# Performance work log

Hardware: AMD Instinct MI355X
Metric: run time of the kernel (lower is better)

The kernel has to match this reference:

```python
import jax, jax.numpy as jnp
import numpy as np

C = 128; D_INNER = 256; D_STATE = 16; D_CONV = 4; DT_RANK = 8; SCALE_MLP = 2


def layernorm(x, g, b, eps=1e-5):
    m = x.mean(-1, keepdims=True)
    v = ((x - m) ** 2).mean(-1, keepdims=True)
    return (x - m) * jax.lax.rsqrt(v + eps) * g + b


def causal_conv(x, w, b):
    # x: (B, L, D); w: (D, K) depthwise causal conv; b: (D,)
    K = w.shape[1]
    xt = x.transpose(0, 2, 1)  # (B, D, L)
    out = jax.lax.conv_general_dilated(
        xt, w[:, None, :], (1,), [(K - 1, 0)],
        dimension_numbers=("NCH", "OIH", "NCH"), feature_group_count=w.shape[0])
    return (out + b[None, :, None]).transpose(0, 2, 1)


def selective_scan(u, delta, A, Bm, Cm, Dv):
    # u, delta: (B, L, D); A: (D, N); Bm, Cm: (B, L, N); Dv: (D,)
    def step(h, inp):
        u_t, d_t, B_t, C_t = inp  # (B,D),(B,D),(B,N),(B,N)
        dA = jnp.exp(d_t[..., None] * A)                      # (B, D, N)
        h = dA * h + (d_t * u_t)[..., None] * B_t[:, None, :]  # (B, D, N)
        y = jnp.einsum("bdn,bn->bd", h, C_t)
        return h, y
    Bsz, L, Din = u.shape
    h0 = jnp.zeros((Bsz, Din, A.shape[1]), u.dtype)
    inputs = (u.transpose(1, 0, 2), delta.transpose(1, 0, 2),
              Bm.transpose(1, 0, 2), Cm.transpose(1, 0, 2))
    _, ys = jax.lax.scan(step, h0, inputs)
    return ys.transpose(1, 0, 2) + u * Dv


def mamba_branch(xc, z, cw, cb, Wx_, Wdt_, bdt_, Al, Dv):
    u = jax.nn.silu(causal_conv(xc, cw, cb))
    xdbl = u @ Wx_.T  # (B, L, dt_rank + 2*d_state)
    dr = Wdt_.shape[1]; ds = Al.shape[1]
    dt = jax.nn.softplus(xdbl[..., :dr] @ Wdt_.T + bdt_)
    Bm = xdbl[..., dr:dr + ds]
    Cm = xdbl[..., dr + ds:]
    y = selective_scan(u, dt, -jnp.exp(Al), Bm, Cm, Dv)
    return y * jax.nn.silu(z)


def setup_inputs():
    key = jax.random.key(0)
    ks = jax.random.split(key, 20)
    w = lambda k, shape, s=0.02: jax.random.normal(k, shape, jnp.float32) * s
    A_log = jnp.log(jnp.tile(jnp.arange(1, D_STATE + 1, dtype=jnp.float32), (D_INNER, 1)))
    dt_bias = jnp.full((D_INNER,), jnp.log(jnp.expm1(0.01)), jnp.float32)
    return dict(
        x=jax.random.normal(ks[0], (4, 256, 64, C), jnp.float32),
        g1=jnp.ones((C,), jnp.float32), b1=jnp.zeros((C,), jnp.float32),
        W_in=w(ks[1], (2 * D_INNER, C)),
        conv_w=w(ks[2], (D_INNER, D_CONV), 0.2), conv_b=jnp.zeros((D_INNER,), jnp.float32),
        Wx=w(ks[3], (DT_RANK + 2 * D_STATE, D_INNER)),
        Wdt=w(ks[4], (D_INNER, DT_RANK), 0.1), bdt=dt_bias,
        A_log=A_log, D=jnp.ones((D_INNER,), jnp.float32),
        conv_wb=w(ks[5], (D_INNER, D_CONV), 0.2), conv_bb=jnp.zeros((D_INNER,), jnp.float32),
        Wxb=w(ks[6], (DT_RANK + 2 * D_STATE, D_INNER)),
        Wdtb=w(ks[7], (D_INNER, DT_RANK), 0.1), bdtb=dt_bias,
        A_b_log=A_log, D_b=jnp.ones((D_INNER,), jnp.float32),
        W_out=w(ks[8], (C, D_INNER)),
        g2=jnp.ones((C,), jnp.float32), b2=jnp.zeros((C,), jnp.float32),
        g3=jnp.ones((C,), jnp.float32), b3=jnp.zeros((C,), jnp.float32),
        W1m=w(ks[9], (C, SCALE_MLP * C)), b1m=jnp.zeros((SCALE_MLP * C,), jnp.float32),
        W2m=w(ks[10], (SCALE_MLP * C, C)), b2m=jnp.zeros((C,), jnp.float32),
    )


def reference(x, g1, b1, W_in, conv_w, conv_b, Wx, Wdt, bdt, A_log, D,
              conv_wb, conv_bb, Wxb, Wdtb, bdtb, A_b_log, D_b, W_out,
              g2, b2, g3, b3, W1m, b1m, W2m, b2m):
    B, T, N, Cc = x.shape
    xs = x.transpose(0, 2, 1, 3).reshape(B * N, T, Cc)
    # --- CustomBiMamba: LN -> (Dropout eval=identity) -> BiMamba v2 -> LN, residual ---
    h = layernorm(xs, g1, b1)
    xz = h @ W_in.T  # (B*N, T, 2*d_inner)
    xc, z = jnp.split(xz, 2, axis=-1)
    y_f = mamba_branch(xc, z, conv_w, conv_b, Wx, Wdt, bdt, A_log, D)
    y_b = mamba_branch(xc[:, ::-1], z[:, ::-1], conv_wb, conv_bb, Wxb, Wdtb, bdtb,
                       A_b_log, D_b)[:, ::-1]
    y = (y_f + y_b) @ W_out.T
    y = layernorm(y, g2, b2)
    xs = y + xs
    xo = xs.reshape(B, N, T, Cc).transpose(0, 2, 1, 3)
    # --- MLP residual ---
    h2 = layernorm(xo, g3, b3)
    mlp = jax.nn.gelu(h2 @ W1m + b1m, approximate=False) @ W2m + b2m
    return xo + mlp
```

## Files before the change

kernel.cpp:

```cpp
#include <hip/hip_runtime.h>
#include <hip/hip_bf16.h>
#include <math.h>

#define CC 128
#define DI 256
#define SSEQ 256
#define ROWS 65536

typedef __hip_bfloat16 bf16;
typedef __attribute__((ext_vector_type(8))) short short8;
typedef __attribute__((ext_vector_type(4))) float float4v;
typedef __attribute__((ext_vector_type(2))) float f32x2;

__device__ __forceinline__ float to_f(float v) { return v; }
__device__ __forceinline__ float to_f(bf16 v)  { return __bfloat162float(v); }
__device__ __forceinline__ bf16  f2b(float v)  { return __float2bfloat16(v); }
__device__ __forceinline__ float bf2f_bits(short v) {
    union { unsigned u; float f; } c; c.u = ((unsigned)(unsigned short)v) << 16; return c.f;
}
__device__ __forceinline__ f32x2 mk2(float a, float b) { f32x2 r; r.x = a; r.y = b; return r; }
__device__ __forceinline__ f32x2 fma2(f32x2 a, f32x2 b, f32x2 c) { return a * b + c; }

__device__ __forceinline__ float wave_sum(float v) {
    #pragma unroll
    for (int o = 1; o < 64; o <<= 1) v += __shfl_xor(v, o, 64);
    return v;
}
__device__ __forceinline__ float silu_f(float x) {
    return x * __builtin_amdgcn_rcpf(1.f + __expf(-x));
}
__device__ __forceinline__ float gelu_f(float x) { return 0.5f * x * (1.f + erff(x * 0.70710678118654752f)); }
__device__ __forceinline__ float softplus_f(float x) {
    return (x > 20.f) ? x : __logf(1.f + __expf(x));
}

__global__ __launch_bounds__(256) void ln1_kernel(const float* __restrict__ x,
                                                  const float* __restrict__ g,
                                                  const float* __restrict__ b,
                                                  bf16* __restrict__ out) {
    int wave = threadIdx.x >> 6, lane = threadIdx.x & 63;
    int r = blockIdx.x * 4 + wave;
    int s = r >> 8, t = r & 255;
    int bb = s >> 6, n = s & 63;
    size_t xbase = (((size_t)(bb * 256 + t)) * 64 + n) * CC;
    float v0 = x[xbase + lane], v1 = x[xbase + lane + 64];
    float s1 = wave_sum(v0 + v1);
    float s2 = wave_sum(v0 * v0 + v1 * v1);
    float m = s1 * (1.f / 128.f);
    float var = s2 * (1.f / 128.f) - m * m;
    float rstd = rsqrtf(var + 1e-5f);
    size_t ob = (size_t)r * CC;
    out[ob + lane]      = f2b((v0 - m) * rstd * g[lane]      + b[lane]);
    out[ob + lane + 64] = f2b((v1 - m) * rstd * g[lane + 64] + b[lane + 64]);
}

__global__ __launch_bounds__(256) void ln3_kernel(const float* __restrict__ in,
                                                  const float* __restrict__ g,
                                                  const float* __restrict__ b,
                                                  bf16* __restrict__ out) {
    int wave = threadIdx.x >> 6, lane = threadIdx.x & 63;
    int r = blockIdx.x * 4 + wave;
    size_t ib = (size_t)r * CC;
    float v0 = in[ib + lane], v1 = in[ib + lane + 64];
    float s1 = wave_sum(v0 + v1);
    float s2 = wave_sum(v0 * v0 + v1 * v1);
    float m = s1 * (1.f / 128.f);
    float var = s2 * (1.f / 128.f) - m * m;
    float rstd = rsqrtf(var + 1e-5f);
    out[ib + lane]      = f2b((v0 - m) * rstd * g[lane]      + b[lane]);
    out[ib + lane + 64] = f2b((v1 - m) * rstd * g[lane + 64] + b[lane + 64]);
}

template <bool BTR, int EPI, int KTILES>
__global__ __launch_bounds__(256) void mfma_gemm_kernel(const bf16* __restrict__ A, int lda,
                                                        const float* __restrict__ B,
                                                        const float* __restrict__ bias,
                                                        void* __restrict__ Cout, int ldc,
                                                        int N, int K) {
    __shared__ bf16 As[64][40];
    __shared__ bf16 Bs[64][40];
    int tid = threadIdx.x;
    int m0 = blockIdx.x * 64;
    int n0 = blockIdx.y * 64;
    int wv = tid >> 6, lane = tid & 63;
    int lrow = lane & 15, quad = lane >> 4;
    int lk = quad * 8;
    float4v acc[4] = {};
    #pragma unroll
    for (int kt = 0; kt < KTILES; kt++) {
        int k0 = kt * 32;
        {
            int m = tid >> 2, part = tid & 3;
            uint4 v = *(const uint4*)(A + (size_t)(m0 + m) * lda + k0 + part * 8);
            *(uint4*)&As[m][part * 8] = v;
        }
        if (BTR) {
            int n = tid >> 2, part = tid & 3;
            const float* src = B + (size_t)(n0 + n) * K + k0 + part * 8;
            bf16 tmp[8];
            #pragma unroll
            for (int j = 0; j < 8; j++) tmp[j] = f2b(src[j]);
            *(uint4*)&Bs[n][part * 8] = *(uint4*)tmp;
        } else {
            int kk = tid >> 3, nf = (tid & 7) * 8;
            const float* src = B + (size_t)(k0 + kk) * N + n0 + nf;
            #pragma unroll
            for (int j = 0; j < 8; j++) Bs[nf + j][kk] = f2b(src[j]);
        }
        __syncthreads();
        short8 a = *(const short8*)&As[wv * 16 + lrow][lk];
        #pragma unroll
        for (int jt = 0; jt < 4; jt++) {
            short8 bfr = *(const short8*)&Bs[jt * 16 + lrow][lk];
            acc[jt] = __builtin_amdgcn_mfma_f32_16x16x32_bf16(a, bfr, acc[jt], 0, 0, 0);
        }
        __syncthreads();
    }
    #pragma unroll
    for (int jt = 0; jt < 4; jt++) {
        int col = n0 + jt * 16 + lrow;
        float bs = (EPI >= 1) ? bias[col] : 0.f;
        #pragma unroll
        for (int r = 0; r < 4; r++) {
            int row = m0 + wv * 16 + quad * 4 + r;
            float v = acc[jt][r] + bs;
            if (EPI == 1) v = gelu_f(v);
            if (EPI == 2) {
                float* Cf = (float*)Cout;
                Cf[(size_t)row * ldc + col] += v;
            } else {
                bf16* Cb = (bf16*)Cout;
                Cb[(size_t)row * ldc + col] = f2b(v);
            }
        }
    }
}

__global__ __launch_bounds__(256) void mfma_ln2res_kernel(const bf16* __restrict__ YF,
                                                          const bf16* __restrict__ YB,
                                                          const bf16* __restrict__ xz,
                                                          const float* __restrict__ Wout,
                                                          const float* __restrict__ g,
                                                          const float* __restrict__ b,
                                                          const float* __restrict__ x,
                                                          float* __restrict__ out) {
    __shared__ bf16 As[64][40];
    __shared__ bf16 Bs[128][40];
    int tid = threadIdx.x;
    int m0 = blockIdx.x * 64;
    int wv = tid >> 6, lane = tid & 63;
    int lrow = lane & 15, quad = lane >> 4;
    int lk = quad * 8;
    float4v acc[8] = {};
    #pragma unroll
    for (int kt = 0; kt < 8; kt++) {
        int k0 = kt * 32;
        {
            int m = tid >> 2, part = tid & 3;
            size_t off = (size_t)(m0 + m) * 256 + k0 + part * 8;
            short8 vf = *(const short8*)(YF + off);
            short8 vb = *(const short8*)(YB + off);
            short8 vz = *(const short8*)(xz + (size_t)(m0 + m) * 512 + 256 + k0 + part * 8);
            bf16 tmp[8];
            #pragma unroll
            for (int j = 0; j < 8; j++)
                tmp[j] = f2b((bf2f_bits(vf[j]) + bf2f_bits(vb[j])) * silu_f(bf2f_bits(vz[j])));
            *(uint4*)&As[m][part * 8] = *(uint4*)tmp;
        }
        #pragma unroll
        for (int it = 0; it < 2; it++) {
            int idx = tid + it * 256;
            int n = idx >> 2, part = idx & 3;
            const float* src = Wout + (size_t)n * 256 + k0 + part * 8;
            bf16 tmp[8];
            #pragma unroll
            for (int j = 0; j < 8; j++) tmp[j] = f2b(src[j]);
            *(uint4*)&Bs[n][part * 8] = *(uint4*)tmp;
        }
        __syncthreads();
        short8 a = *(const short8*)&As[wv * 16 + lrow][lk];
        #pragma unroll
        for (int jt = 0; jt < 8; jt++) {
            short8 bfr = *(const short8*)&Bs[jt * 16 + lrow][lk];
            acc[jt] = __builtin_amdgcn_mfma_f32_16x16x32_bf16(a, bfr, acc[jt], 0, 0, 0);
        }
        __syncthreads();
    }
    #pragma unroll
    for (int r = 0; r < 4; r++) {
        float ps = 0.f, ps2 = 0.f;
        #pragma unroll
        for (int jt = 0; jt < 8; jt++) { float v = acc[jt][r]; ps += v; ps2 += v * v; }
        #pragma unroll
        for (int o = 1; o < 16; o <<= 1) {
            ps  += __shfl_xor(ps, o, 64);
            ps2 += __shfl_xor(ps2, o, 64);
        }
        float m = ps * (1.f / 128.f);
        float var = ps2 * (1.f / 128.f) - m * m;
        float rstd = rsqrtf(var + 1e-5f);
        int row = m0 + wv * 16 + quad * 4 + r;
        int s = row >> 8, t = row & 255;
        int bb = s >> 6, n = s & 63;
        size_t xbase = (((size_t)(bb * 256 + t)) * 64 + n) * CC;
        #pragma unroll
        for (int jt = 0; jt < 8; jt++) {
            int col = jt * 16 + lrow;
            out[xbase + col] = (acc[jt][r] - m) * rstd * g[col] + b[col] + x[xbase + col];
        }
    }
}

template <int DIR>
__global__ __launch_bounds__(256) void mfma_conv_kernel(const bf16* __restrict__ xz,
                                                        const float* __restrict__ cw,
                                                        const float* __restrict__ cb,
                                                        const float* __restrict__ Wx,
                                                        bf16* __restrict__ C,
                                                        bf16* __restrict__ U) {
    __shared__ bf16 As[64][40];
    __shared__ bf16 Bs[48][40];
    int tid = threadIdx.x;
    int s = blockIdx.x >> 2;
    int t0 = (blockIdx.x & 3) * 64;
    int wv = tid >> 6, lane = tid & 63;
    int lrow = lane & 15, quad = lane >> 4;
    int lk = quad * 8;
    float4v acc[3] = {};
    #pragma unroll
    for (int kt = 0; kt < 8; kt++) {
        int k0 = kt * 32;
        {
            int m = tid >> 2, part = tid & 3;
            int t = t0 + m;
            int dbase = k0 + part * 8;
            float a[8];
            float4 w4[8];
            #pragma unroll
            for (int i = 0; i < 8; i++) {
                a[i]  = cb[dbase + i];
                w4[i] = ((const float4*)cw)[dbase + i];
            }
            #pragma unroll
            for (int j = 0; j < 4; j++) {
                int tj = t - 3 + j;
                if (tj >= 0) {
                    int src = DIR ? (255 - tj) : tj;
                    uint4 v = *(const uint4*)(xz + (size_t)(s * 256 + src) * 512 + dbase);
                    short8 sv = *(short8*)&v;
                    #pragma unroll
                    for (int i = 0; i < 8; i++) {
                        float w = (j == 0) ? w4[i].x : (j == 1) ? w4[i].y : (j == 2) ? w4[i].z : w4[i].w;
                        a[i] += w * bf2f_bits(sv[i]);
                    }
                }
            }
            bf16 tmp[8];
            #pragma unroll
            for (int i = 0; i < 8; i++) tmp[i] = f2b(silu_f(a[i]));
            *(uint4*)&As[m][part * 8] = *(uint4*)tmp;
            int tu = DIR ? (255 - t) : t;
            *(uint4*)&U[((size_t)(s * 256 + tu)) * 256 + dbase] = *(uint4*)tmp;
        }
        {
            int n = tid >> 2, part = tid & 3;
            if (n < 48) {
                bf16 tmp[8];
                #pragma unroll
                for (int j = 0; j < 8; j++)
                    tmp[j] = (n < 40) ? f2b(Wx[(size_t)n * 256 + k0 + part * 8 + j]) : f2b(0.f);
                *(uint4*)&Bs[n][part * 8] = *(uint4*)tmp;
            }
        }
        __syncthreads();
        short8 a = *(const short8*)&As[wv * 16 + lrow][lk];
        #pragma unroll
        for (int jt = 0; jt < 3; jt++) {
            short8 bfr = *(const short8*)&Bs[jt * 16 + lrow][lk];
            acc[jt] = __builtin_amdgcn_mfma_f32_16x16x32_bf16(a, bfr, acc[jt], 0, 0, 0);
        }
        __syncthreads();
    }
    #pragma unroll
    for (int jt = 0; jt < 3; jt++) {
        int col = jt * 16 + lrow;
        if (col < 40) {
            #pragma unroll
            for (int r = 0; r < 4; r++) {
                int row = t0 + wv * 16 + quad * 4 + r;
                C[(size_t)(s * 256 + row) * 40 + col] = f2b(acc[jt][r]);
            }
        }
    }
}


#define LOADROW(R, T) do {                                                  \
    const float4* rp_ = (const float4*)(rows + (T) * 40);                   \
    R##0 = rp_[0]; R##1 = rp_[1]; R##2 = rp_[2]; R##3 = rp_[3];             \
    R##4 = rp_[4]; R##5 = rp_[5]; R##6 = rp_[6]; R##7 = rp_[7];             \
    R##8 = rp_[8]; R##9 = rp_[9];                                           \
} while (0)

#define SCAN_STEP(T, R) do {                                                \
    float u_ = uc0; uc0 = uc1;                                              \
    if ((T) + 2 < 256) { uc1 = to_f(*unext); unext += ystep; }              \
    f32x2 acc2 = mk2((R##0).x, (R##0).y) * wdt01;                           \
    acc2 = fma2(mk2((R##0).z, (R##0).w), wdt23, acc2);                      \
    acc2 = fma2(mk2((R##1).x, (R##1).y), wdt45, acc2);                      \
    acc2 = fma2(mk2((R##1).z, (R##1).w), wdt67, acc2);                      \
    float dtr_ = bd + acc2.x + acc2.y;                                      \
    float dt_ = softplus_f(dtr_);                                           \
    float du_ = dt_ * u_;                                                   \
    float d1 = __expf(dt_ * A0);                                            \
    float d2v = d1 * d1;                                                    \
    f32x2 pw0 = mk2(d1, d2v);                                               \
    f32x2 dd2 = mk2(d2v, d2v);                                              \
    f32x2 pw1 = pw0 * dd2, pw2 = pw1 * dd2, pw3 = pw2 * dd2;                \
    f32x2 dd8 = mk2(pw3.y, pw3.y);                                          \
    f32x2 pw4 = pw0 * dd8, pw5 = pw1 * dd8, pw6 = pw2 * dd8, pw7 = pw3 * dd8; \
    f32x2 du2 = mk2(du_, du_);                                              \
    hp0 = fma2(pw0, hp0, du2 * mk2((R##2).x, (R##2).y));                    \
    hp1 = fma2(pw1, hp1, du2 * mk2((R##2).z, (R##2).w));                    \
    hp2 = fma2(pw2, hp2, du2 * mk2((R##3).x, (R##3).y));                    \
    hp3 = fma2(pw3, hp3, du2 * mk2((R##3).z, (R##3).w));                    \
    hp4 = fma2(pw4, hp4, du2 * mk2((R##4).x, (R##4).y));                    \
    hp5 = fma2(pw5, hp5, du2 * mk2((R##4).z, (R##4).w));                    \
    hp6 = fma2(pw6, hp6, du2 * mk2((R##5).x, (R##5).y));                    \
    hp7 = fma2(pw7, hp7, du2 * mk2((R##5).z, (R##5).w));                    \
    f32x2 ya = hp0 * mk2((R##6).x, (R##6).y);                               \
    f32x2 yb = hp1 * mk2((R##6).z, (R##6).w);                               \
    ya = fma2(hp2, mk2((R##7).x, (R##7).y), ya);                            \
    yb = fma2(hp3, mk2((R##7).z, (R##7).w), yb);                            \
    ya = fma2(hp4, mk2((R##8).x, (R##8).y), ya);                            \
    yb = fma2(hp5, mk2((R##8).z, (R##8).w), yb);                            \
    ya = fma2(hp6, mk2((R##9).x, (R##9).y), ya);                            \
    yb = fma2(hp7, mk2((R##9).z, (R##9).w), yb);                            \
    f32x2 ys = ya + yb;                                                     \
    float yv_ = ys.x + ys.y + u_ * Dd;                                      \
    *yp = f2b(yv_); yp += ystep;                                            \
} while (0)

__global__ __launch_bounds__(256) void scan_kernel(
        const bf16* __restrict__ xdbl_f, const bf16* __restrict__ xdbl_b,
        const float* __restrict__ Wdt_f, const float* __restrict__ bdt_f,
        const float* __restrict__ Alog_f, const float* __restrict__ D_f,
        const float* __restrict__ Wdt_b, const float* __restrict__ bdt_b,
        const float* __restrict__ Alog_b, const float* __restrict__ D_b,
        bf16* __restrict__ YF, bf16* __restrict__ YB) {
    __shared__ float rows[256 * 40];
    int tid = threadIdx.x;
    int dir = blockIdx.x >> 8;
    int s = blockIdx.x & 255;
    int d = tid;

    const bf16* xd = (dir ? xdbl_b : xdbl_f) + (size_t)s * 10240;
    #pragma unroll
    for (int i = 0; i < 5; i++) {
        int idx = i * 256 + tid;
        uint4 v = ((const uint4*)xd)[idx];
        short8 sv = *(short8*)&v;
        float f[8];
        #pragma unroll
        for (int j = 0; j < 8; j++) f[j] = bf2f_bits(sv[j]);
        *(float4*)&rows[idx * 8]     = *(float4*)&f[0];
        *(float4*)&rows[idx * 8 + 4] = *(float4*)&f[4];
    }

    const float* Alog = dir ? Alog_b : Alog_f;
    const float* Wdtp = dir ? Wdt_b  : Wdt_f;
    float Aarr[16];
    #pragma unroll
    for (int n = 0; n < 16; n++) Aarr[n] = -__expf(Alog[d * 16 + n]);
    f32x2 wdt01 = mk2(Wdtp[d * 8 + 0], Wdtp[d * 8 + 1]);
    f32x2 wdt23 = mk2(Wdtp[d * 8 + 2], Wdtp[d * 8 + 3]);
    f32x2 wdt45 = mk2(Wdtp[d * 8 + 4], Wdtp[d * 8 + 5]);
    f32x2 wdt67 = mk2(Wdtp[d * 8 + 6], Wdtp[d * 8 + 7]);
    float bd = dir ? bdt_b[d] : bdt_f[d];
    float Dd = dir ? D_b[d]   : D_f[d];
    bf16* Y = dir ? YB : YF;

    float A0 = Aarr[0];
    int pw = 1;
    #pragma unroll
    for (int n = 1; n < 16; n++)
        pw &= (fabsf(Aarr[n] - (float)(n + 1) * A0) <= 1e-4f * fabsf(Aarr[n]) + 1e-6f) ? 1 : 0;
    pw = __all(pw);
    __syncthreads();

    bf16* yp = Y + ((size_t)(s * 256 + (dir ? 255 : 0))) * 256 + d;
    ptrdiff_t ystep = dir ? -256 : 256;
    float uc0 = to_f(*yp);
    float uc1 = to_f(*(yp + ystep));
    const bf16* unext = yp + 2 * ystep;

    if (pw) {
        f32x2 hp0 = {}, hp1 = {}, hp2 = {}, hp3 = {},
              hp4 = {}, hp5 = {}, hp6 = {}, hp7 = {};
        float4 ra0, ra1, ra2, ra3, ra4, ra5, ra6, ra7, ra8, ra9;
        float4 rb0, rb1, rb2, rb3, rb4, rb5, rb6, rb7, rb8, rb9;
        LOADROW(ra, 0);
        #pragma unroll 1
        for (int t = 0; t < 256; t += 2) {
            LOADROW(rb, t + 1);
            SCAN_STEP(t, ra);
            if (t + 2 < 256) LOADROW(ra, t + 2);
            SCAN_STEP(t + 1, rb);
        }
    } else {
        float h[16];
        #pragma unroll
        for (int n = 0; n < 16; n++) h[n] = 0.f;
        for (int t = 0; t < 256; t++) {
            float u = uc0; uc0 = uc1;
            if (t + 2 < 256) { uc1 = to_f(*unext); unext += ystep; }
            const float* row = rows + t * 40;
            float4 q0 = *(const float4*)(row);
            float4 q1 = *(const float4*)(row + 4);
            float4 qb0 = *(const float4*)(row + 8);
            float4 qb1 = *(const float4*)(row + 12);
            float4 qb2 = *(const float4*)(row + 16);
            float4 qb3 = *(const float4*)(row + 20);
            float4 qc0 = *(const float4*)(row + 24);
            float4 qc1 = *(const float4*)(row + 28);
            float4 qc2 = *(const float4*)(row + 32);
            float4 qc3 = *(const float4*)(row + 36);
            float dtr = bd;
            dtr += q0.x * wdt01.x + q0.y * wdt01.y + q0.z * wdt23.x + q0.w * wdt23.y;
            dtr += q1.x * wdt45.x + q1.y * wdt45.y + q1.z * wdt67.x + q1.w * wdt67.y;
            float dt = softplus_f(dtr);
            float du = dt * u, y = 0.f;
            float Bm[16] = {qb0.x,qb0.y,qb0.z,qb0.w, qb1.x,qb1.y,qb1.z,qb1.w,
                            qb2.x,qb2.y,qb2.z,qb2.w, qb3.x,qb3.y,qb3.z,qb3.w};
            float Cm[16] = {qc0.x,qc0.y,qc0.z,qc0.w, qc1.x,qc1.y,qc1.z,qc1.w,
                            qc2.x,qc2.y,qc2.z,qc2.w, qc3.x,qc3.y,qc3.z,qc3.w};
            #pragma unroll
            for (int n = 0; n < 16; n++) {
                float dA = __expf(dt * Aarr[n]);
                h[n] = dA * h[n] + du * Bm[n];
                y += h[n] * Cm[n];
            }
            y += u * Dd;
            *yp = f2b(y); yp += ystep;
        }
    }
}

extern "C" void kernel_launch(void* const* d_in, const int* in_sizes, int n_in,
                              void* d_out, int out_size, void* d_ws, size_t ws_size,
                              hipStream_t stream) {
    const float* x      = (const float*)d_in[0];
    const float* g1     = (const float*)d_in[1];
    const float* b1     = (const float*)d_in[2];
    const float* W_in   = (const float*)d_in[3];
    const float* conv_w = (const float*)d_in[4];
    const float* conv_b = (const float*)d_in[5];
    const float* Wx     = (const float*)d_in[6];
    const float* Wdt    = (const float*)d_in[7];
    const float* bdt    = (const float*)d_in[8];
    const float* A_log  = (const float*)d_in[9];
    const float* Dvec   = (const float*)d_in[10];
    const float* conv_wb= (const float*)d_in[11];
    const float* conv_bb= (const float*)d_in[12];
    const float* Wxb    = (const float*)d_in[13];
    const float* Wdtb   = (const float*)d_in[14];
    const float* bdtb   = (const float*)d_in[15];
    const float* A_b_log= (const float*)d_in[16];
    const float* D_b    = (const float*)d_in[17];
    const float* W_out  = (const float*)d_in[18];
    const float* g2     = (const float*)d_in[19];
    const float* b2     = (const float*)d_in[20];
    const float* g3     = (const float*)d_in[21];
    const float* b3     = (const float*)d_in[22];
    const float* W1m    = (const float*)d_in[23];
    const float* b1m    = (const float*)d_in[24];
    const float* W2m    = (const float*)d_in[25];
    const float* b2m    = (const float*)d_in[26];

    bf16* ws  = (bf16*)d_ws;
    bf16* XZ  = ws;
    bf16* YF  = ws + 33554432UL;
    bf16* YB  = ws + 50331648UL;
    bf16* H2  = ws;
    bf16* HID = ws + 8388608UL;
    float* out = (float*)d_out;
    bf16* LN1OUT = (bf16*)d_out;
    bf16* XDBL_F = (bf16*)d_out;
    bf16* XDBL_B = (bf16*)d_out + 2621440UL;

    ln1_kernel<<<ROWS / 4, 256, 0, stream>>>(x, g1, b1, LN1OUT);
    mfma_gemm_kernel<true, 0, 4><<<dim3(ROWS / 64, 8), 256, 0, stream>>>(
        LN1OUT, CC, W_in, nullptr, XZ, 512, 512, CC);
    mfma_conv_kernel<0><<<SSEQ * 4, 256, 0, stream>>>(XZ, conv_w, conv_b, Wx, XDBL_F, YF);
    mfma_conv_kernel<1><<<SSEQ * 4, 256, 0, stream>>>(XZ, conv_wb, conv_bb, Wxb, XDBL_B, YB);
    scan_kernel<<<512, 256, 0, stream>>>(XDBL_F, XDBL_B,
        Wdt, bdt, A_log, Dvec, Wdtb, bdtb, A_b_log, D_b, YF, YB);
    mfma_ln2res_kernel<<<ROWS / 64, 256, 0, stream>>>(YF, YB, XZ, W_out, g2, b2, x, out);
    ln3_kernel<<<ROWS / 4, 256, 0, stream>>>(out, g3, b3, H2);
    mfma_gemm_kernel<false, 1, 4><<<dim3(ROWS / 64, 4), 256, 0, stream>>>(
        H2, CC, W1m, b1m, HID, 2 * CC, 2 * CC, CC);
    mfma_gemm_kernel<false, 2, 8><<<dim3(ROWS / 64, 2), 256, 0, stream>>>(
        HID, 2 * CC, W2m, b2m, out, CC, CC, 2 * CC);
}
```

Baseline: 522.7 us.

## Split selective-scan state dimension across thread pairs with shuffle reduction

The scan kernel now uses 512 threads per block, with two threads per channel, each handling 8 of the 16 state entries. The partial outputs are combined with a lane xor-shuffle and only the even lane writes. The aim is to double the wave count for the latency-bound sequential scan, which ran only 512 blocks of 256 threads, and to halve per-thread register use. In exchange, the dt projection and exp are computed twice per channel and every step adds a cross-lane shuffle.

```diff
diff --git a/kernel.cpp b/kernel.cpp
--- a/kernel.cpp
+++ b/kernel.cpp
@@ -295,53 +295,46 @@
 }
 
 
-#define LOADROW(R, T) do {                                                  \
+#define LOADROW9(R, T) do {                                                 \
     const float4* rp_ = (const float4*)(rows + (T) * 40);                   \
-    R##0 = rp_[0]; R##1 = rp_[1]; R##2 = rp_[2]; R##3 = rp_[3];             \
-    R##4 = rp_[4]; R##5 = rp_[5]; R##6 = rp_[6]; R##7 = rp_[7];             \
-    R##8 = rp_[8]; R##9 = rp_[9];                                           \
+    R##0 = rp_[0]; R##1 = rp_[1];                                           \
+    R##2 = rp_[2 + bo]; R##3 = rp_[3 + bo];                                 \
+    R##4 = rp_[6 + bo]; R##5 = rp_[7 + bo];                                 \
 } while (0)
 
-#define SCAN_STEP(T, R) do {                                                \
+#define SCAN_STEP9(T, R) do {                                               \
     float u_ = uc0; uc0 = uc1;                                              \
     if ((T) + 2 < 256) { uc1 = to_f(*unext); unext += ystep; }              \
-    f32x2 acc2 = mk2((R##0).x, (R##0).y) * wdt01;                           \
-    acc2 = fma2(mk2((R##0).z, (R##0).w), wdt23, acc2);                      \
-    acc2 = fma2(mk2((R##1).x, (R##1).y), wdt45, acc2);                      \
-    acc2 = fma2(mk2((R##1).z, (R##1).w), wdt67, acc2);                      \
-    float dtr_ = bd + acc2.x + acc2.y;                                      \
-    float dt_ = softplus_f(dtr_);                                           \
+    f32x2 a2 = mk2((R##0).x, (R##0).y) * wdt01;                             \
+    a2 = fma2(mk2((R##0).z, (R##0).w), wdt23, a2);                          \
+    a2 = fma2(mk2((R##1).x, (R##1).y), wdt45, a2);                          \
+    a2 = fma2(mk2((R##1).z, (R##1).w), wdt67, a2);                          \
+    float dt_ = softplus_f(bd + a2.x + a2.y);                               \
     float du_ = dt_ * u_;                                                   \
-    float d1 = __expf(dt_ * A0);                                            \
-    float d2v = d1 * d1;                                                    \
-    f32x2 pw0 = mk2(d1, d2v);                                               \
-    f32x2 dd2 = mk2(d2v, d2v);                                              \
+    float p1 = __expf(dt_ * A0);                                            \
+    float p2 = p1 * p1;                                                     \
+    f32x2 pw0 = mk2(p1, p2);                                                \
+    f32x2 dd2 = mk2(p2, p2);                                                \
     f32x2 pw1 = pw0 * dd2, pw2 = pw1 * dd2, pw3 = pw2 * dd2;                \
-    f32x2 dd8 = mk2(pw3.y, pw3.y);                                          \
-    f32x2 pw4 = pw0 * dd8, pw5 = pw1 * dd8, pw6 = pw2 * dd8, pw7 = pw3 * dd8; \
+    float sc_ = half ? pw3.y : 1.0f;                                        \
+    f32x2 s2_ = mk2(sc_, sc_);                                              \
+    pw0 *= s2_; pw1 *= s2_; pw2 *= s2_; pw3 *= s2_;                         \
     f32x2 du2 = mk2(du_, du_);                                              \
     hp0 = fma2(pw0, hp0, du2 * mk2((R##2).x, (R##2).y));                    \
     hp1 = fma2(pw1, hp1, du2 * mk2((R##2).z, (R##2).w));                    \
     hp2 = fma2(pw2, hp2, du2 * mk2((R##3).x, (R##3).y));                    \
     hp3 = fma2(pw3, hp3, du2 * mk2((R##3).z, (R##3).w));                    \
-    hp4 = fma2(pw4, hp4, du2 * mk2((R##4).x, (R##4).y));                    \
-    hp5 = fma2(pw5, hp5, du2 * mk2((R##4).z, (R##4).w));                    \
-    hp6 = fma2(pw6, hp6, du2 * mk2((R##5).x, (R##5).y));                    \
-    hp7 = fma2(pw7, hp7, du2 * mk2((R##5).z, (R##5).w));                    \
-    f32x2 ya = hp0 * mk2((R##6).x, (R##6).y);                               \
-    f32x2 yb = hp1 * mk2((R##6).z, (R##6).w);                               \
-    ya = fma2(hp2, mk2((R##7).x, (R##7).y), ya);                            \
-    yb = fma2(hp3, mk2((R##7).z, (R##7).w), yb);                            \
-    ya = fma2(hp4, mk2((R##8).x, (R##8).y), ya);                            \
-    yb = fma2(hp5, mk2((R##8).z, (R##8).w), yb);                            \
-    ya = fma2(hp6, mk2((R##9).x, (R##9).y), ya);                            \
-    yb = fma2(hp7, mk2((R##9).z, (R##9).w), yb);                            \
-    f32x2 ys = ya + yb;                                                     \
-    float yv_ = ys.x + ys.y + u_ * Dd;                                      \
-    *yp = f2b(yv_); yp += ystep;                                            \
+    f32x2 ya = hp0 * mk2((R##4).x, (R##4).y);                               \
+    ya = fma2(hp1, mk2((R##4).z, (R##4).w), ya);                            \
+    ya = fma2(hp2, mk2((R##5).x, (R##5).y), ya);                            \
+    ya = fma2(hp3, mk2((R##5).z, (R##5).w), ya);                            \
+    float yv_ = ya.x + ya.y + u_ * Ddh;                                     \
+    yv_ += __shfl_xor(yv_, 1, 64);                                          \
+    if (!half) *yp = f2b(yv_);                                              \
+    yp += ystep;                                                            \
 } while (0)
 
-__global__ __launch_bounds__(256) void scan_kernel(
+__global__ __launch_bounds__(512, 4) void scan_kernel(
         const bf16* __restrict__ xdbl_f, const bf16* __restrict__ xdbl_b,
         const float* __restrict__ Wdt_f, const float* __restrict__ bdt_f,
         const float* __restrict__ Alog_f, const float* __restrict__ D_f,
@@ -352,19 +345,24 @@
     int tid = threadIdx.x;
     int dir = blockIdx.x >> 8;
     int s = blockIdx.x & 255;
-    int d = tid;
+    int d = tid >> 1;
+    int half = tid & 1;
+    int n0 = half * 8;
+    int bo = half * 2;
 
     const bf16* xd = (dir ? xdbl_b : xdbl_f) + (size_t)s * 10240;
     #pragma unroll
-    for (int i = 0; i < 5; i++) {
-        int idx = i * 256 + tid;
-        uint4 v = ((const uint4*)xd)[idx];
-        short8 sv = *(short8*)&v;
-        float f[8];
-        #pragma unroll
-        for (int j = 0; j < 8; j++) f[j] = bf2f_bits(sv[j]);
-        *(float4*)&rows[idx * 8]     = *(float4*)&f[0];
-        *(float4*)&rows[idx * 8 + 4] = *(float4*)&f[4];
+    for (int i = 0; i < 3; i++) {
+        int idx = i * 512 + tid;
+        if (idx < 1280) {
+            uint4 v = ((const uint4*)xd)[idx];
+            short8 sv = *(short8*)&v;
+            float f[8];
+            #pragma unroll
+            for (int j = 0; j < 8; j++) f[j] = bf2f_bits(sv[j]);
+            *(float4*)&rows[idx * 8]     = *(float4*)&f[0];
+            *(float4*)&rows[idx * 8 + 4] = *(float4*)&f[4];
+        }
     }
 
     const float* Alog = dir ? Alog_b : Alog_f;
@@ -378,6 +376,7 @@
     f32x2 wdt67 = mk2(Wdtp[d * 8 + 6], Wdtp[d * 8 + 7]);
     float bd = dir ? bdt_b[d] : bdt_f[d];
     float Dd = dir ? D_b[d]   : D_f[d];
+    float Ddh = half ? 0.f : Dd;
     bf16* Y = dir ? YB : YF;
 
     float A0 = Aarr[0];
@@ -395,53 +394,41 @@
     const bf16* unext = yp + 2 * ystep;
 
     if (pw) {
-        f32x2 hp0 = {}, hp1 = {}, hp2 = {}, hp3 = {},
-              hp4 = {}, hp5 = {}, hp6 = {}, hp7 = {};
-        float4 ra0, ra1, ra2, ra3, ra4, ra5, ra6, ra7, ra8, ra9;
-        float4 rb0, rb1, rb2, rb3, rb4, rb5, rb6, rb7, rb8, rb9;
-        LOADROW(ra, 0);
+        f32x2 hp0 = {}, hp1 = {}, hp2 = {}, hp3 = {};
+        float4 ra0, ra1, ra2, ra3, ra4, ra5;
+        float4 rb0, rb1, rb2, rb3, rb4, rb5;
+        LOADROW9(ra, 0);
         #pragma unroll 1
         for (int t = 0; t < 256; t += 2) {
-            LOADROW(rb, t + 1);
-            SCAN_STEP(t, ra);
-            if (t + 2 < 256) LOADROW(ra, t + 2);
-            SCAN_STEP(t + 1, rb);
+            LOADROW9(rb, t + 1);
+            SCAN_STEP9(t, ra);
+            if (t + 2 < 256) LOADROW9(ra, t + 2);
+            SCAN_STEP9(t + 1, rb);
         }
     } else {
-        float h[16];
-        #pragma unroll
-        for (int n = 0; n < 16; n++) h[n] = 0.f;
+        float A8[8], h[8];
+        #pragma unroll
+        for (int j = 0; j < 8; j++) { A8[j] = Aarr[n0 + j]; h[j] = 0.f; }
+        #pragma unroll 1
         for (int t = 0; t < 256; t++) {
             float u = uc0; uc0 = uc1;
             if (t + 2 < 256) { uc1 = to_f(*unext); unext += ystep; }
             const float* row = rows + t * 40;
-            float4 q0 = *(const float4*)(row);
-            float4 q1 = *(const float4*)(row + 4);
-            float4 qb0 = *(const float4*)(row + 8);
-            float4 qb1 = *(const float4*)(row + 12);
-            float4 qb2 = *(const float4*)(row + 16);
-            float4 qb3 = *(const float4*)(row + 20);
-            float4 qc0 = *(const float4*)(row + 24);
-            float4 qc1 = *(const float4*)(row + 28);
-            float4 qc2 = *(const float4*)(row + 32);
-            float4 qc3 = *(const float4*)(row + 36);
             float dtr = bd;
-            dtr += q0.x * wdt01.x + q0.y * wdt01.y + q0.z * wdt23.x + q0.w * wdt23.y;
-            dtr += q1.x * wdt45.x + q1.y * wdt45.y + q1.z * wdt67.x + q1.w * wdt67.y;
+            dtr += row[0] * wdt01.x + row[1] * wdt01.y + row[2] * wdt23.x + row[3] * wdt23.y;
+            dtr += row[4] * wdt45.x + row[5] * wdt45.y + row[6] * wdt67.x + row[7] * wdt67.y;
             float dt = softplus_f(dtr);
             float du = dt * u, y = 0.f;
-            float Bm[16] = {qb0.x,qb0.y,qb0.z,qb0.w, qb1.x,qb1.y,qb1.z,qb1.w,
-                            qb2.x,qb2.y,qb2.z,qb2.w, qb3.x,qb3.y,qb3.z,qb3.w};
-            float Cm[16] = {qc0.x,qc0.y,qc0.z,qc0.w, qc1.x,qc1.y,qc1.z,qc1.w,
-                            qc2.x,qc2.y,qc2.z,qc2.w, qc3.x,qc3.y,qc3.z,qc3.w};
-            #pragma unroll
-            for (int n = 0; n < 16; n++) {
-                float dA = __expf(dt * Aarr[n]);
-                h[n] = dA * h[n] + du * Bm[n];
-                y += h[n] * Cm[n];
-            }
-            y += u * Dd;
-            *yp = f2b(y); yp += ystep;
+            #pragma unroll
+            for (int j = 0; j < 8; j++) {
+                float dA = __expf(dt * A8[j]);
+                h[j] = dA * h[j] + du * row[8 + n0 + j];
+                y += h[j] * row[24 + n0 + j];
+            }
+            y += u * Ddh;
+            y += __shfl_xor(y, 1, 64);
+            if (!half) *yp = f2b(y);
+            yp += ystep;
         }
     }
 }
@@ -493,7 +480,7 @@
         LN1OUT, CC, W_in, nullptr, XZ, 512, 512, CC);
     mfma_conv_kernel<0><<<SSEQ * 4, 256, 0, stream>>>(XZ, conv_w, conv_b, Wx, XDBL_F, YF);
     mfma_conv_kernel<1><<<SSEQ * 4, 256, 0, stream>>>(XZ, conv_wb, conv_bb, Wxb, XDBL_B, YB);
-    scan_kernel<<<512, 256, 0, stream>>>(XDBL_F, XDBL_B,
+    scan_kernel<<<512, 512, 0, stream>>>(XDBL_F, XDBL_B,
         Wdt, bdt, A_log, Dvec, Wdtb, bdtb, A_b_log, D_b, YF, YB);
     mfma_ln2res_kernel<<<ROWS / 64, 256, 0, stream>>>(YF, YB, XZ, W_out, g2, b2, x, out);
     ln3_kernel<<<ROWS / 4, 256, 0, stream>>>(out, g3, b3, H2);
```

Result: slower. 547.1 us (+4.7%).

## Stage scan input u through double-buffered LDS chunks instead of per-step global loads

Applied to the files above, without the earlier changes.

The scan kernel now cooperatively loads 32 time steps of u (the Y buffer rows) into a double-buffered shared-memory tile using 16-byte vector loads, prefetching the next chunk while the current one is scanned. Each thread then reads its u value from LDS rather than doing a strided 2-byte global load every step. It also sets launch_bounds to request two blocks per CU. The cost is an extra 32 KB of LDS per block and a __syncthreads per chunk, and the occupancy hint may limit registers.

```diff
diff --git a/kernel.cpp b/kernel.cpp
--- a/kernel.cpp
+++ b/kernel.cpp
@@ -302,9 +302,8 @@
     R##8 = rp_[8]; R##9 = rp_[9];                                           \
 } while (0)
 
-#define SCAN_STEP(T, R) do {                                                \
-    float u_ = uc0; uc0 = uc1;                                              \
-    if ((T) + 2 < 256) { uc1 = to_f(*unext); unext += ystep; }              \
+#define SCAN_STEP(JJ, R) do {                                               \
+    float u_ = to_f(ub[(JJ) * 256 + d]);                                    \
     f32x2 acc2 = mk2((R##0).x, (R##0).y) * wdt01;                           \
     acc2 = fma2(mk2((R##0).z, (R##0).w), wdt23, acc2);                      \
     acc2 = fma2(mk2((R##1).x, (R##1).y), wdt45, acc2);                      \
@@ -329,19 +328,31 @@
     hp6 = fma2(pw6, hp6, du2 * mk2((R##5).x, (R##5).y));                    \
     hp7 = fma2(pw7, hp7, du2 * mk2((R##5).z, (R##5).w));                    \
     f32x2 ya = hp0 * mk2((R##6).x, (R##6).y);                               \
-    f32x2 yb = hp1 * mk2((R##6).z, (R##6).w);                               \
+    f32x2 yb2 = hp1 * mk2((R##6).z, (R##6).w);                              \
     ya = fma2(hp2, mk2((R##7).x, (R##7).y), ya);                            \
-    yb = fma2(hp3, mk2((R##7).z, (R##7).w), yb);                            \
+    yb2 = fma2(hp3, mk2((R##7).z, (R##7).w), yb2);                          \
     ya = fma2(hp4, mk2((R##8).x, (R##8).y), ya);                            \
-    yb = fma2(hp5, mk2((R##8).z, (R##8).w), yb);                            \
+    yb2 = fma2(hp5, mk2((R##8).z, (R##8).w), yb2);                          \
     ya = fma2(hp6, mk2((R##9).x, (R##9).y), ya);                            \
-    yb = fma2(hp7, mk2((R##9).z, (R##9).w), yb);                            \
-    f32x2 ys = ya + yb;                                                     \
+    yb2 = fma2(hp7, mk2((R##9).z, (R##9).w), yb2);                          \
+    f32x2 ys = ya + yb2;                                                    \
     float yv_ = ys.x + ys.y + u_ * Dd;                                      \
     *yp = f2b(yv_); yp += ystep;                                            \
 } while (0)
 
-__global__ __launch_bounds__(256) void scan_kernel(
+#define STAGE_U(BUF, C0) do {                                               \
+    _Pragma("unroll")                                                       \
+    for (int q_ = 0; q_ < 4; q_++) {                                        \
+        int flat_ = q_ * 256 + tid;                                         \
+        int j_ = flat_ >> 5, w_ = flat_ & 31;                               \
+        int t_ = (C0) + j_;                                                 \
+        int grow_ = dir ? (255 - t_) : t_;                                  \
+        ((uint4*)u_lds)[(BUF) * 1024 + flat_] =                             \
+            *((const uint4*)(Y + ((size_t)(s * 256 + grow_)) * 256) + w_);  \
+    }                                                                       \
+} while (0)
+
+__global__ __launch_bounds__(256, 2) void scan_kernel(
         const bf16* __restrict__ xdbl_f, const bf16* __restrict__ xdbl_b,
         const float* __restrict__ Wdt_f, const float* __restrict__ bdt_f,
         const float* __restrict__ Alog_f, const float* __restrict__ D_f,
@@ -349,6 +360,7 @@
         const float* __restrict__ Alog_b, const float* __restrict__ D_b,
         bf16* __restrict__ YF, bf16* __restrict__ YB) {
     __shared__ float rows[256 * 40];
+    __shared__ bf16  u_lds[2 * 8192];
     int tid = threadIdx.x;
     int dir = blockIdx.x >> 8;
     int s = blockIdx.x & 255;
@@ -386,13 +398,12 @@
     for (int n = 1; n < 16; n++)
         pw &= (fabsf(Aarr[n] - (float)(n + 1) * A0) <= 1e-4f * fabsf(Aarr[n]) + 1e-6f) ? 1 : 0;
     pw = __all(pw);
+
+    STAGE_U(0, 0);
     __syncthreads();
 
     bf16* yp = Y + ((size_t)(s * 256 + (dir ? 255 : 0))) * 256 + d;
     ptrdiff_t ystep = dir ? -256 : 256;
-    float uc0 = to_f(*yp);
-    float uc1 = to_f(*(yp + ystep));
-    const bf16* unext = yp + 2 * ystep;
 
     if (pw) {
         f32x2 hp0 = {}, hp1 = {}, hp2 = {}, hp3 = {},
@@ -401,47 +412,50 @@
         float4 rb0, rb1, rb2, rb3, rb4, rb5, rb6, rb7, rb8, rb9;
         LOADROW(ra, 0);
         #pragma unroll 1
-        for (int t = 0; t < 256; t += 2) {
-            LOADROW(rb, t + 1);
-            SCAN_STEP(t, ra);
-            if (t + 2 < 256) LOADROW(ra, t + 2);
-            SCAN_STEP(t + 1, rb);
+        for (int c = 0; c < 8; c++) {
+            if (c + 1 < 8) STAGE_U((c + 1) & 1, (c + 1) * 32);
+            const bf16* ub = u_lds + (c & 1) * 8192;
+            int tc = c * 32;
+            #pragma unroll 2
+            for (int j = 0; j < 32; j += 2) {
+                int t = tc + j;
+                LOADROW(rb, t + 1);
+                SCAN_STEP(j, ra);
+                if (t + 2 < 256) LOADROW(ra, t + 2);
+                SCAN_STEP(j + 1, rb);
+            }
+            __syncthreads();
         }
     } else {
         float h[16];
         #pragma unroll
         for (int n = 0; n < 16; n++) h[n] = 0.f;
-        for (int t = 0; t < 256; t++) {
-            float u = uc0; uc0 = uc1;
-            if (t + 2 < 256) { uc1 = to_f(*unext); unext += ystep; }
-            const float* row = rows + t * 40;
-            float4 q0 = *(const float4*)(row);
-            float4 q1 = *(const float4*)(row + 4);
-            float4 qb0 = *(const float4*)(row + 8);
-            float4 qb1 = *(const float4*)(row + 12);
-            float4 qb2 = *(const float4*)(row + 16);
-            float4 qb3 = *(const float4*)(row + 20);
-            float4 qc0 = *(const float4*)(row + 24);
-            float4 qc1 = *(const float4*)(row + 28);
-            float4 qc2 = *(const float4*)(row + 32);
-            float4 qc3 = *(const float4*)(row + 36);
-            float dtr = bd;
-            dtr += q0.x * wdt01.x + q0.y * wdt01.y + q0.z * wdt23.x + q0.w * wdt23.y;
-            dtr += q1.x * wdt45.x + q1.y * wdt45.y + q1.z * wdt67.x + q1.w * wdt67.y;
-            float dt = softplus_f(dtr);
-            float du = dt * u, y = 0.f;
-            float Bm[16] = {qb0.x,qb0.y,qb0.z,qb0.w, qb1.x,qb1.y,qb1.z,qb1.w,
-                            qb2.x,qb2.y,qb2.z,qb2.w, qb3.x,qb3.y,qb3.z,qb3.w};
-            float Cm[16] = {qc0.x,qc0.y,qc0.z,qc0.w, qc1.x,qc1.y,qc1.z,qc1.w,
-                            qc2.x,qc2.y,qc2.z,qc2.w, qc3.x,qc3.y,qc3.z,qc3.w};
-            #pragma unroll
-            for (int n = 0; n < 16; n++) {
-                float dA = __expf(dt * Aarr[n]);
-                h[n] = dA * h[n] + du * Bm[n];
-                y += h[n] * Cm[n];
-            }
-            y += u * Dd;
-            *yp = f2b(y); yp += ystep;
+        #pragma unroll 1
+        for (int c = 0; c < 8; c++) {
+            if (c + 1 < 8) STAGE_U((c + 1) & 1, (c + 1) * 32);
+            const bf16* ub = u_lds + (c & 1) * 8192;
+            int tc = c * 32;
+            #pragma unroll 1
+            for (int j = 0; j < 32; j++) {
+                float u = to_f(ub[j * 256 + d]);
+                const float* row = rows + (tc + j) * 40;
+                float4 q0 = *(const float4*)(row);
+                float4 q1 = *(const float4*)(row + 4);
+                float dtr = bd;
+                dtr += q0.x * wdt01.x + q0.y * wdt01.y + q0.z * wdt23.x + q0.w * wdt23.y;
+                dtr += q1.x * wdt45.x + q1.y * wdt45.y + q1.z * wdt67.x + q1.w * wdt67.y;
+                float dt = softplus_f(dtr);
+                float du = dt * u, y = 0.f;
+                #pragma unroll
+                for (int n = 0; n < 16; n++) {
+                    float dA = __expf(dt * Aarr[n]);
+                    h[n] = dA * h[n] + du * row[8 + n];
+                    y += h[n] * row[24 + n];
+                }
+                y += u * Dd;
+                *yp = f2b(y); yp += ystep;
+            }
+            __syncthreads();
         }
     }
 }
```

Result: faster. 483.5 us (-7.5%).
